# Kernel optimization log

Measured on AMD Instinct MI355X. Metric: run time of the kernel, lower is better.

Reference implementation:

```python
import jax, jax.numpy as jnp
import numpy as np
from jax import lax

B, C, H, W = 8, 64, 96, 96
OC = 64
KH = KW = 3
DG = 1
STRIDE = 1
PAD = 1
DIL = 1


def setup_inputs() -> dict:
    key = jax.random.key(0)
    k1, k2, k3, k4, k5 = jax.random.split(key, 5)
    x = jax.random.normal(k1, (B, C, H, W), jnp.float32)
    off_ch = DG * 3 * KH * KW
    # small random offset/mask conv params (the original inits them to zero,
    # which would make offsets degenerate; small values exercise the sampler)
    w_off = jax.random.normal(k2, (off_ch, C, KH, KW), jnp.float32) * 0.01
    b_off = jax.random.normal(k3, (off_ch,), jnp.float32) * 0.01
    stdv = 1.0 / float(np.sqrt(C * KH * KW))
    weight = jax.random.uniform(k4, (OC, C, KH, KW), jnp.float32, -stdv, stdv)
    bias = jax.random.uniform(k5, (OC,), jnp.float32, -stdv, stdv)
    return {"x": x, "w_off": w_off, "b_off": b_off, "weight": weight, "bias": bias}


def _deform_conv(x, w_off, b_off, weight, bias):
    Bt, Ct, Ht, Wt = x.shape
    K = KH * KW
    # standard conv producing offsets + mask logits
    om = lax.conv_general_dilated(
        x, w_off, (STRIDE, STRIDE), ((PAD, PAD), (PAD, PAD)),
        rhs_dilation=(DIL, DIL), dimension_numbers=("NCHW", "OIHW", "NCHW"),
    ) + b_off[None, :, None, None]
    o1, o2, m = jnp.split(om, 3, axis=1)  # each [B, DG*K, Ho, Wo]
    Ho, Wo = o1.shape[2], o1.shape[3]
    mask = jax.nn.sigmoid(m).reshape(Bt, DG, 1, K, Ho, Wo)
    off_y = o1.reshape(Bt, DG, K, Ho, Wo)
    off_x = o2.reshape(Bt, DG, K, Ho, Wo)
    # base sampling grid: p = out_pos*stride - pad + k*dilation + offset
    kk = jnp.arange(K)
    base_y = (kk // KW)[:, None] * DIL + (jnp.arange(Ho) * STRIDE - PAD)[None, :]  # [K, Ho]
    base_x = (kk % KW)[:, None] * DIL + (jnp.arange(Wo) * STRIDE - PAD)[None, :]   # [K, Wo]
    py = off_y + base_y[None, None, :, :, None].astype(x.dtype)  # [B, DG, K, Ho, Wo]
    px = off_x + base_x[None, None, :, None, :].astype(x.dtype)
    y0 = jnp.floor(py)
    x0 = jnp.floor(px)
    ly = py - y0
    lx = px - x0
    Cg = Ct // DG
    xg = x.reshape(Bt, DG, Cg, Ht * Wt)

    def gath(xf, idx):  # xf [Cg, H*W], idx [K*Ho*Wo]
        return jnp.take(xf, idx, axis=1)

    gather = jax.vmap(jax.vmap(gath))  # over B, DG

    sampled = jnp.zeros((Bt, DG, Cg, K, Ho, Wo), x.dtype)
    for dy, dx, wgt in ((0, 0, (1 - ly) * (1 - lx)), (0, 1, (1 - ly) * lx),
                        (1, 0, ly * (1 - lx)), (1, 1, ly * lx)):
        yy = y0 + dy
        xx = x0 + dx
        valid = (yy >= 0) & (yy < Ht) & (xx >= 0) & (xx < Wt)
        yi = jnp.clip(yy, 0, Ht - 1).astype(jnp.int32)
        xi = jnp.clip(xx, 0, Wt - 1).astype(jnp.int32)
        idx = (yi * Wt + xi).reshape(Bt, DG, K * Ho * Wo)
        v = gather(xg, idx).reshape(Bt, DG, Cg, K, Ho, Wo)
        sampled = sampled + v * (wgt * valid)[:, :, None]
    sampled = sampled * mask  # modulated
    wr = weight.reshape(OC, DG, Cg, K)
    out = jnp.einsum("bgckhw,ogck->bohw", sampled, wr) + bias[None, :, None, None]
    return out


def reference(x, w_off, b_off, weight, bias):
    return _deform_conv(x, w_off, b_off, weight, bias)
```

## Files before the change

### kernel.cpp

```cpp
#include <hip/hip_runtime.h>
#include <math.h>

#define Bn 8
#define Cn 64
#define Hn 96
#define Wn 96
#define HWn (Hn*Wn)
#define OCn 64
#define Kn 9
#define OFFCn 27
#define NPIX (Bn*HWn)
#define PGRPS (NPIX/64)
#define BLK_PER_B (HWn/64)

#define WPK1_N 15552
#define WPK2M_SHORTS 131072
#define WS_DWORDS (45*NPIX + WPK1_N + WPK2M_SHORTS/2)
#define WS_BYTES  ((size_t)WS_DWORDS*4)

typedef __attribute__((ext_vector_type(8))) short short8v;
typedef __attribute__((ext_vector_type(4))) float f32x4;

static __device__ __forceinline__ unsigned short bf16_rne(float f) {
    unsigned int u = __float_as_uint(f);
    return (unsigned short)((u + 0x7FFFu + ((u >> 16) & 1u)) >> 16);
}
static __device__ __forceinline__ float bf16_back(unsigned short h) {
    return __uint_as_float(((unsigned int)h) << 16);
}

__global__ __launch_bounds__(256) void dcn_wprep(
    const float* __restrict__ w_off,
    const float* __restrict__ weight,
    float* __restrict__ wpk1,
    short* __restrict__ wpk2m)
{
    const int g = blockIdx.x * 256 + threadIdx.x;
    if (g < WPK1_N) {
        const int c_all = g / 243;
        const int och   = (g % 243) / 9;
        const int ki    = g % 9;
        wpk1[g] = w_off[(och * 64 + c_all) * 9 + ki];
    }
    if (g < WPK2M_SHORTS / 8) {
        const int lane = g & 63;
        const int oct  = (g >> 6) & 3;
        const int c    = g >> 8;
        const int oc   = oct * 16 + (lane & 15);
        const float* wsrc = weight + (oc * 64 + c) * 9;
        short8v v;
#pragma unroll
        for (int j = 0; j < 8; ++j) {
            const int s = ((lane >> 4) & 3) * 8 + j;
            float f = 0.0f;
            if (s <= 8)                  f = wsrc[s];
            else if (s >= 16 && s <= 24) f = wsrc[s - 16];
            v[j] = (short)bf16_rne(f);
        }
        ((short8v*)wpk2m)[g] = v;
    }
}

__global__ __launch_bounds__(256, 2) void dcn_k1(
    const float* __restrict__ x,
    const float* __restrict__ wpk1,
    const float* __restrict__ b_off,
    float* __restrict__ pwbuf,
    int*   __restrict__ abuf)
{
    __shared__ float lds[4 * 64 * OFFCn];

    const int tid  = threadIdx.x;
    const int lane = tid & 63;
    const int wv   = tid >> 6;
    const int cbase = __builtin_amdgcn_readfirstlane(wv * 16);

    const int bid = (blockIdx.x & 7) * BLK_PER_B + (blockIdx.x >> 3);

    const int p  = bid * 64 + lane;
    const int b  = p / HWn;
    const int hw = p % HWn;
    const int ho = hw / Wn;
    const int wo = hw % Wn;

    const float* xb = x + b * (Cn * HWn);

    int   toff[Kn];
    float tval[Kn];
#pragma unroll
    for (int ki = 0; ki < Kn; ++ki) {
        const int yy = ho + ki / 3 - 1, xx = wo + ki % 3 - 1;
        const bool v = (yy >= 0) && (yy < Hn) && (xx >= 0) && (xx < Wn);
        toff[ki] = min(max(yy, 0), Hn - 1) * Wn + min(max(xx, 0), Wn - 1);
        tval[ki] = v ? 1.0f : 0.0f;
    }

    float om[OFFCn];
#pragma unroll
    for (int j = 0; j < OFFCn; ++j) om[j] = 0.0f;

    const float* wstream = wpk1 + cbase * 243;
    for (int ci = 0; ci < 16; ++ci) {
        const float* xc = xb + (cbase + ci) * HWn;
        float xk[Kn];
#pragma unroll
        for (int ki = 0; ki < Kn; ++ki)
            xk[ki] = xc[toff[ki]] * tval[ki];

        const float* wc = wstream + ci * 243;
#pragma unroll
        for (int och = 0; och < OFFCn; ++och) {
            const float* wp = wc + och * 9;
            float a = om[och];
#pragma unroll
            for (int ki = 0; ki < Kn; ++ki)
                a = fmaf(xk[ki], wp[ki], a);
            om[och] = a;
        }
    }

#pragma unroll
    for (int j = 0; j < OFFCn; ++j)
        lds[(wv * 64 + lane) * OFFCn + j] = om[j];
    __syncthreads();
#pragma unroll
    for (int j = 0; j < OFFCn; ++j) {
        float a = b_off[j];
#pragma unroll
        for (int ww = 0; ww < 4; ++ww)
            a += lds[(ww * 64 + lane) * OFFCn + j];
        om[j] = a;
    }

    float pw0[Kn], pw1[Kn], pw2[Kn], pw3[Kn];
    int   pav[Kn];
#pragma unroll
    for (int ki = 0; ki < Kn; ++ki) {
        const float py = om[ki]      + (float)(ki / 3 + ho - 1);
        const float px = om[Kn + ki] + (float)(ki % 3 + wo - 1);
        const float m  = 1.0f / (1.0f + __expf(-om[2 * Kn + ki]));

        const float y0f = floorf(py), x0f = floorf(px);
        const float ly = py - y0f, lx = px - x0f;
        const int iy0 = (int)y0f, ix0 = (int)x0f;
        const int iy1 = iy0 + 1,  ix1 = ix0 + 1;

        const float vy0 = (iy0 >= 0 && iy0 < Hn) ? 1.0f : 0.0f;
        const float vy1 = (iy1 >= 0 && iy1 < Hn) ? 1.0f : 0.0f;
        const float vx0 = (ix0 >= 0 && ix0 < Wn) ? 1.0f : 0.0f;
        const float vx1 = (ix1 >= 0 && ix1 < Wn) ? 1.0f : 0.0f;

        const int iy0c = min(max(iy0, 0), Hn - 1);
        const int iy1c = min(max(iy1, 0), Hn - 1);
        const int ix0c = min(max(ix0, 0), Wn - 1);
        const int ix1c = min(max(ix1, 0), Wn - 1);

        pw0[ki] = m * (1.0f - ly) * (1.0f - lx) * vy0 * vx0;
        pw1[ki] = m * (1.0f - ly) * lx          * vy0 * vx1;
        pw2[ki] = m * ly          * (1.0f - lx) * vy1 * vx0;
        pw3[ki] = m * ly          * lx          * vy1 * vx1;
        const int pa  = iy0c * Wn + ix0c;
        const int dx  = ix1c - ix0c;
        const int dyw = (iy1c - iy0c) * Wn;
        pav[ki] = pa | (dx << 16) | (dyw << 17);
    }

    if (wv == 0) {
#pragma unroll
        for (int ki = 0; ki < Kn; ++ki) pwbuf[(0 * Kn + ki) * NPIX + p] = pw0[ki];
#pragma unroll
        for (int ki = 0; ki < Kn; ++ki) abuf[ki * NPIX + p] = pav[ki];
    } else if (wv == 1) {
#pragma unroll
        for (int ki = 0; ki < Kn; ++ki) pwbuf[(1 * Kn + ki) * NPIX + p] = pw1[ki];
    } else if (wv == 2) {
#pragma unroll
        for (int ki = 0; ki < Kn; ++ki) pwbuf[(2 * Kn + ki) * NPIX + p] = pw2[ki];
    } else {
#pragma unroll
        for (int ki = 0; ki < Kn; ++ki) pwbuf[(3 * Kn + ki) * NPIX + p] = pw3[ki];
    }
}

__global__ __launch_bounds__(256, 2) void dcn_k2(
    const float* __restrict__ x,
    const short* __restrict__ wpk2m,
    const float* __restrict__ bias,
    const float* __restrict__ pwbuf,
    const int*   __restrict__ abuf,
    float* __restrict__ out)
{
    __shared__ short smp[32 * 64 * 8];

    const int tid  = threadIdx.x;
    const int lane = tid & 63;
    const int wv   = tid >> 6;

    const int bid = (blockIdx.x & 7) * BLK_PER_B + (blockIdx.x >> 3);

    const int p0  = bid * 64;
    const int b   = p0 / HWn;
    const int hwb = p0 % HWn;
    const int p   = p0 + lane;

    const float* xb = x + b * (Cn * HWn);

    float pw0[Kn], pw1[Kn], pw2[Kn], pw3[Kn];
    int   pav[Kn];
#pragma unroll
    for (int ki = 0; ki < Kn; ++ki) pw0[ki] = pwbuf[(0 * Kn + ki) * NPIX + p];
#pragma unroll
    for (int ki = 0; ki < Kn; ++ki) pw1[ki] = pwbuf[(1 * Kn + ki) * NPIX + p];
#pragma unroll
    for (int ki = 0; ki < Kn; ++ki) pw2[ki] = pwbuf[(2 * Kn + ki) * NPIX + p];
#pragma unroll
    for (int ki = 0; ki < Kn; ++ki) pw3[ki] = pwbuf[(3 * Kn + ki) * NPIX + p];
#pragma unroll
    for (int ki = 0; ki < Kn; ++ki) pav[ki] = abuf[ki * NPIX + p];

    f32x4 acc[4];
#pragma unroll
    for (int oct = 0; oct < 4; ++oct) acc[oct] = (f32x4){0.f, 0.f, 0.f, 0.f};

    const short8v* afrags = (const short8v*)wpk2m;

    for (int chunk = 0; chunk < 8; ++chunk) {
#pragma unroll
        for (int cc = 0; cc < 2; ++cc) {
            const int cl = (wv << 1) | cc;
            const float* xc = xb + (chunk * 8 + cl) * HWn;
            unsigned short hi[Kn], lo[Kn];
#pragma unroll
            for (int ki = 0; ki < Kn; ++ki) {
                const int av  = pav[ki];
                const int pa  = av & 0xFFFF;
                const int dx  = (av >> 16) & 1;
                const int dyw = av >> 17;
                const float* bp = xc + pa;
                const float v = pw0[ki] * bp[0] + pw1[ki] * bp[dx]
                              + pw2[ki] * bp[dyw] + pw3[ki] * bp[dyw + dx];
                hi[ki] = bf16_rne(v);
                lo[ki] = bf16_rne(v - bf16_back(hi[ki]));
            }
            short8v h0, h1, l0, l1;
#pragma unroll
            for (int j = 0; j < 8; ++j) { h0[j] = (short)hi[j]; l0[j] = (short)lo[j]; }
            h1 = (short8v){(short)hi[8], 0, 0, 0, 0, 0, 0, 0};
            l1 = (short8v){(short)lo[8], 0, 0, 0, 0, 0, 0, 0};
            const int r0 = cl * 4;
            *(short8v*)&smp[((r0 + 0) * 64 + lane) * 8] = h0;
            *(short8v*)&smp[((r0 + 1) * 64 + lane) * 8] = h1;
            *(short8v*)&smp[((r0 + 2) * 64 + lane) * 8] = l0;
            *(short8v*)&smp[((r0 + 3) * 64 + lane) * 8] = l1;
        }
        __syncthreads();

#pragma unroll
        for (int ks = 0; ks < 8; ++ks) {
            const short8v bfrag = *(const short8v*)
                &smp[((ks * 4 + (lane >> 4)) * 64 + wv * 16 + (lane & 15)) * 8];
#pragma unroll
            for (int oct = 0; oct < 4; ++oct) {
                const short8v afrag =
                    afrags[(((chunk * 8 + ks) * 4) + oct) * 64 + lane];
                acc[oct] = __builtin_amdgcn_mfma_f32_16x16x32_bf16(
                    afrag, bfrag, acc[oct], 0, 0, 0);
            }
        }
        __syncthreads();
    }

    const int pxl = wv * 16 + (lane & 15);
    float* ob = out + b * (OCn * HWn) + hwb + pxl;
#pragma unroll
    for (int oct = 0; oct < 4; ++oct) {
#pragma unroll
        for (int r = 0; r < 4; ++r) {
            const int oc = oct * 16 + ((lane >> 4) & 3) * 4 + r;
            ob[oc * HWn] = acc[oct][r] + bias[oc];
        }
    }
}

__global__ __launch_bounds__(64) void dcn_r1(
    const float* __restrict__ x,
    const float* __restrict__ w_off,
    const float* __restrict__ b_off,
    const float* __restrict__ weight,
    const float* __restrict__ bias,
    float* __restrict__ out)
{
    const int p  = blockIdx.x * 64 + threadIdx.x;
    const int b  = p / HWn;
    const int hw = p % HWn;
    const int ho = hw / Wn;
    const int wo = hw % Wn;
    const float* xb = x + b * (Cn * HWn);

    float om[OFFCn];
#pragma unroll
    for (int j = 0; j < OFFCn; ++j) om[j] = b_off[j];

    int   toff[Kn];
    float tval[Kn];
#pragma unroll
    for (int ki = 0; ki < Kn; ++ki) {
        const int yy = ho + ki / 3 - 1, xx = wo + ki % 3 - 1;
        const bool v = (yy >= 0) && (yy < Hn) && (xx >= 0) && (xx < Wn);
        toff[ki] = min(max(yy, 0), Hn - 1) * Wn + min(max(xx, 0), Wn - 1);
        tval[ki] = v ? 1.0f : 0.0f;
    }
    for (int c = 0; c < Cn; ++c) {
        const float* xc = xb + c * HWn;
        float xk[Kn];
#pragma unroll
        for (int ki = 0; ki < Kn; ++ki) xk[ki] = xc[toff[ki]] * tval[ki];
        const float* wc = w_off + c * Kn;
#pragma unroll
        for (int och = 0; och < OFFCn; ++och) {
            const float* wp = wc + och * (Cn * Kn);
            float a = om[och];
#pragma unroll
            for (int ki = 0; ki < Kn; ++ki) a = fmaf(xk[ki], wp[ki], a);
            om[och] = a;
        }
    }
    float pw0[Kn], pw1[Kn], pw2[Kn], pw3[Kn];
    int   pa[Kn], pdx[Kn], pdyw[Kn];
#pragma unroll
    for (int ki = 0; ki < Kn; ++ki) {
        const float py = om[ki]      + (float)(ki / 3 + ho - 1);
        const float px = om[Kn + ki] + (float)(ki % 3 + wo - 1);
        const float m  = 1.0f / (1.0f + __expf(-om[2 * Kn + ki]));
        const float y0f = floorf(py), x0f = floorf(px);
        const float ly = py - y0f, lx = px - x0f;
        const int iy0 = (int)y0f, ix0 = (int)x0f;
        const int iy1 = iy0 + 1,  ix1 = ix0 + 1;
        const float vy0 = (iy0 >= 0 && iy0 < Hn) ? 1.0f : 0.0f;
        const float vy1 = (iy1 >= 0 && iy1 < Hn) ? 1.0f : 0.0f;
        const float vx0 = (ix0 >= 0 && ix0 < Wn) ? 1.0f : 0.0f;
        const float vx1 = (ix1 >= 0 && ix1 < Wn) ? 1.0f : 0.0f;
        const int iy0c = min(max(iy0, 0), Hn - 1);
        const int iy1c = min(max(iy1, 0), Hn - 1);
        const int ix0c = min(max(ix0, 0), Wn - 1);
        const int ix1c = min(max(ix1, 0), Wn - 1);
        pw0[ki] = m * (1.0f - ly) * (1.0f - lx) * vy0 * vx0;
        pw1[ki] = m * (1.0f - ly) * lx          * vy0 * vx1;
        pw2[ki] = m * ly          * (1.0f - lx) * vy1 * vx0;
        pw3[ki] = m * ly          * lx          * vy1 * vx1;
        pa[ki]   = iy0c * Wn + ix0c;
        pdx[ki]  = ix1c - ix0c;
        pdyw[ki] = (iy1c - iy0c) * Wn;
    }
    float acc[OCn];
#pragma unroll
    for (int oc = 0; oc < OCn; ++oc) acc[oc] = bias[oc];
    for (int c = 0; c < Cn; ++c) {
        const float* xc = xb + c * HWn;
        float s[Kn];
#pragma unroll
        for (int ki = 0; ki < Kn; ++ki) {
            const float* bp = xc + pa[ki];
            s[ki] = pw0[ki] * bp[0] + pw1[ki] * bp[pdx[ki]]
                  + pw2[ki] * bp[pdyw[ki]] + pw3[ki] * bp[pdyw[ki] + pdx[ki]];
        }
        const float* wc = weight + c * Kn;
#pragma unroll
        for (int oc = 0; oc < OCn; ++oc) {
            const float* wp = wc + oc * (Cn * Kn);
            float a = acc[oc];
#pragma unroll
            for (int ki = 0; ki < Kn; ++ki) a = fmaf(s[ki], wp[ki], a);
            acc[oc] = a;
        }
    }
    float* ob = out + b * (OCn * HWn) + hw;
#pragma unroll
    for (int oc = 0; oc < OCn; ++oc) ob[oc * HWn] = acc[oc];
}

extern "C" void kernel_launch(void* const* d_in, const int* in_sizes, int n_in,
                              void* d_out, int out_size, void* d_ws, size_t ws_size,
                              hipStream_t stream) {
    const float* x      = (const float*)d_in[0];
    const float* w_off  = (const float*)d_in[1];
    const float* b_off  = (const float*)d_in[2];
    const float* weight = (const float*)d_in[3];
    const float* bias   = (const float*)d_in[4];
    float* out = (float*)d_out;

    if (ws_size >= WS_BYTES) {
        float* pwbuf = (float*)d_ws;
        int*   abuf  = (int*)((float*)d_ws + 36 * NPIX);
        float* wpk1  = (float*)d_ws + 45 * NPIX;
        short* wpk2m = (short*)(wpk1 + WPK1_N);
        hipLaunchKernelGGL(dcn_wprep, dim3(64), dim3(256), 0, stream,
                           w_off, weight, wpk1, wpk2m);
        hipLaunchKernelGGL(dcn_k1, dim3(PGRPS), dim3(256), 0, stream,
                           x, wpk1, b_off, pwbuf, abuf);
        hipLaunchKernelGGL(dcn_k2, dim3(PGRPS), dim3(256), 0, stream,
                           x, wpk2m, bias, pwbuf, abuf, out);
    } else {
        hipLaunchKernelGGL(dcn_r1, dim3(NPIX / 64), dim3(64), 0, stream,
                           x, w_off, b_off, weight, bias, out);
    }
}
```

Measured before the change: 237.3 us.

## Restructure deform-conv GEMM kernel to per-wave private LDS tiles without block barriers

```diff
diff --git a/kernel.cpp b/kernel.cpp
--- a/kernel.cpp
+++ b/kernel.cpp
@@ -19,6 +19,7 @@
 #define WS_BYTES  ((size_t)WS_DWORDS*4)
 
 typedef __attribute__((ext_vector_type(8))) short short8v;
+typedef __attribute__((ext_vector_type(4))) short short4v;
 typedef __attribute__((ext_vector_type(4))) float f32x4;
 
 static __device__ __forceinline__ unsigned short bf16_rne(float f) {
@@ -182,7 +183,7 @@
     }
 }
 
-__global__ __launch_bounds__(256, 2) void dcn_k2(
+__global__ __launch_bounds__(128, 2) void dcn_k2w(
     const float* __restrict__ x,
     const short* __restrict__ wpk2m,
     const float* __restrict__ bias,
@@ -190,94 +191,147 @@
     const int*   __restrict__ abuf,
     float* __restrict__ out)
 {
-    __shared__ short smp[32 * 64 * 8];
+    __shared__ short smp[2 * 2 * 2048];
 
     const int tid  = threadIdx.x;
     const int lane = tid & 63;
     const int wv   = tid >> 6;
+    const int q    = lane >> 5;
+    const int px   = lane & 31;
+    const int kb   = q * 4;
 
     const int bid = (blockIdx.x & 7) * BLK_PER_B + (blockIdx.x >> 3);
-
-    const int p0  = bid * 64;
+    const int p0  = bid * 64 + wv * 32;
     const int b   = p0 / HWn;
     const int hwb = p0 % HWn;
-    const int p   = p0 + lane;
+    const int p   = p0 + px;
 
     const float* xb = x + b * (Cn * HWn);
-
-    float pw0[Kn], pw1[Kn], pw2[Kn], pw3[Kn];
-    int   pav[Kn];
-#pragma unroll
-    for (int ki = 0; ki < Kn; ++ki) pw0[ki] = pwbuf[(0 * Kn + ki) * NPIX + p];
-#pragma unroll
-    for (int ki = 0; ki < Kn; ++ki) pw1[ki] = pwbuf[(1 * Kn + ki) * NPIX + p];
-#pragma unroll
-    for (int ki = 0; ki < Kn; ++ki) pw2[ki] = pwbuf[(2 * Kn + ki) * NPIX + p];
-#pragma unroll
-    for (int ki = 0; ki < Kn; ++ki) pw3[ki] = pwbuf[(3 * Kn + ki) * NPIX + p];
-#pragma unroll
-    for (int ki = 0; ki < Kn; ++ki) pav[ki] = abuf[ki * NPIX + p];
-
-    f32x4 acc[4];
-#pragma unroll
-    for (int oct = 0; oct < 4; ++oct) acc[oct] = (f32x4){0.f, 0.f, 0.f, 0.f};
+    short* myA = smp + wv * 4096;
+    short* myB = myA + 2048;
+
+    {
+        short8v z = (short8v){0, 0, 0, 0, 0, 0, 0, 0};
+#pragma unroll
+        for (int t = 0; t < 2; ++t) {
+            const int idx = t * 64 + lane;
+            const int r   = 1 + 2 * (idx >> 5);
+            const int pp  = idx & 31;
+            *(short8v*)&myA[(r * 32 + pp) * 8] = z;
+            *(short8v*)&myB[(r * 32 + pp) * 8] = z;
+        }
+    }
+
+    float pw0[5], pw1[5], pw2[5], pw3[5];
+    int   pav[5];
+#pragma unroll
+    for (int i = 0; i < 5; ++i) pw0[i] = pwbuf[(0 * Kn + kb + i) * NPIX + p];
+#pragma unroll
+    for (int i = 0; i < 5; ++i) pw1[i] = pwbuf[(1 * Kn + kb + i) * NPIX + p];
+#pragma unroll
+    for (int i = 0; i < 5; ++i) pw2[i] = pwbuf[(2 * Kn + kb + i) * NPIX + p];
+#pragma unroll
+    for (int i = 0; i < 5; ++i) pw3[i] = pwbuf[(3 * Kn + kb + i) * NPIX + p];
+#pragma unroll
+    for (int i = 0; i < 5; ++i) pav[i] = abuf[(kb + i) * NPIX + p];
+
+    f32x4 acc[2][4];
+#pragma unroll
+    for (int t = 0; t < 2; ++t)
+#pragma unroll
+        for (int oct = 0; oct < 4; ++oct)
+            acc[t][oct] = (f32x4){0.f, 0.f, 0.f, 0.f};
 
     const short8v* afrags = (const short8v*)wpk2m;
-
-    for (int chunk = 0; chunk < 8; ++chunk) {
-#pragma unroll
-        for (int cc = 0; cc < 2; ++cc) {
-            const int cl = (wv << 1) | cc;
-            const float* xc = xb + (chunk * 8 + cl) * HWn;
-            unsigned short hi[Kn], lo[Kn];
-#pragma unroll
-            for (int ki = 0; ki < Kn; ++ki) {
-                const int av  = pav[ki];
+    const int r4  = lane >> 4;
+    const int c16 = lane & 15;
+
+    for (int it = 0; it < 16; ++it) {
+        const int ch0 = it * 4;
+
+#pragma unroll
+        for (int c = 0; c < 2; ++c) {
+            const float* xc = xb + (ch0 + c) * HWn;
+            unsigned short h[5], l[5];
+#pragma unroll
+            for (int i = 0; i < 5; ++i) {
+                const int av  = pav[i];
                 const int pa  = av & 0xFFFF;
                 const int dx  = (av >> 16) & 1;
                 const int dyw = av >> 17;
                 const float* bp = xc + pa;
-                const float v = pw0[ki] * bp[0] + pw1[ki] * bp[dx]
-                              + pw2[ki] * bp[dyw] + pw3[ki] * bp[dyw + dx];
-                hi[ki] = bf16_rne(v);
-                lo[ki] = bf16_rne(v - bf16_back(hi[ki]));
+                const float v = pw0[i] * bp[0] + pw1[i] * bp[dx]
+                              + pw2[i] * bp[dyw] + pw3[i] * bp[dyw + dx];
+                h[i] = bf16_rne(v);
+                l[i] = bf16_rne(v - bf16_back(h[i]));
             }
-            short8v h0, h1, l0, l1;
-#pragma unroll
-            for (int j = 0; j < 8; ++j) { h0[j] = (short)hi[j]; l0[j] = (short)lo[j]; }
-            h1 = (short8v){(short)hi[8], 0, 0, 0, 0, 0, 0, 0};
-            l1 = (short8v){(short)lo[8], 0, 0, 0, 0, 0, 0, 0};
-            const int r0 = cl * 4;
-            *(short8v*)&smp[((r0 + 0) * 64 + lane) * 8] = h0;
-            *(short8v*)&smp[((r0 + 1) * 64 + lane) * 8] = h1;
-            *(short8v*)&smp[((r0 + 2) * 64 + lane) * 8] = l0;
-            *(short8v*)&smp[((r0 + 3) * 64 + lane) * 8] = l1;
-        }
-        __syncthreads();
-
-#pragma unroll
-        for (int ks = 0; ks < 8; ++ks) {
-            const short8v bfrag = *(const short8v*)
-                &smp[((ks * 4 + (lane >> 4)) * 64 + wv * 16 + (lane & 15)) * 8];
+            short4v h4 = (short4v){(short)h[0], (short)h[1], (short)h[2], (short)h[3]};
+            short4v l4 = (short4v){(short)l[0], (short)l[1], (short)l[2], (short)l[3]};
+            *(short4v*)&myA[((c * 4 + 0) * 32 + px) * 8 + q * 4] = h4;
+            *(short4v*)&myA[((c * 4 + 2) * 32 + px) * 8 + q * 4] = l4;
+            myA[((c * 4 + 0 + q) * 32 + px) * 8 + (q ? 0 : 4)] = (short)h[4];
+            myA[((c * 4 + 2 + q) * 32 + px) * 8 + (q ? 0 : 4)] = (short)l[4];
+        }
+
+#pragma unroll
+        for (int c = 0; c < 2; ++c) {
+            const float* xc = xb + (ch0 + 2 + c) * HWn;
+            unsigned short h[5], l[5];
+#pragma unroll
+            for (int i = 0; i < 5; ++i) {
+                const int av  = pav[i];
+                const int pa  = av & 0xFFFF;
+                const int dx  = (av >> 16) & 1;
+                const int dyw = av >> 17;
+                const float* bp = xc + pa;
+                const float v = pw0[i] * bp[0] + pw1[i] * bp[dx]
+                              + pw2[i] * bp[dyw] + pw3[i] * bp[dyw + dx];
+                h[i] = bf16_rne(v);
+                l[i] = bf16_rne(v - bf16_back(h[i]));
+            }
+            short4v h4 = (short4v){(short)h[0], (short)h[1], (short)h[2], (short)h[3]};
+            short4v l4 = (short4v){(short)l[0], (short)l[1], (short)l[2], (short)l[3]};
+            *(short4v*)&myB[((c * 4 + 0) * 32 + px) * 8 + q * 4] = h4;
+            *(short4v*)&myB[((c * 4 + 2) * 32 + px) * 8 + q * 4] = l4;
+            myB[((c * 4 + 0 + q) * 32 + px) * 8 + (q ? 0 : 4)] = (short)h[4];
+            myB[((c * 4 + 2 + q) * 32 + px) * 8 + (q ? 0 : 4)] = (short)l[4];
+        }
+
+#pragma unroll
+        for (int c = 0; c < 2; ++c) {
+            const short8v bf0 = *(const short8v*)&myA[((c * 4 + r4) * 32 + c16) * 8];
+            const short8v bf1 = *(const short8v*)&myA[((c * 4 + r4) * 32 + 16 + c16) * 8];
 #pragma unroll
             for (int oct = 0; oct < 4; ++oct) {
-                const short8v afrag =
-                    afrags[(((chunk * 8 + ks) * 4) + oct) * 64 + lane];
-                acc[oct] = __builtin_amdgcn_mfma_f32_16x16x32_bf16(
-                    afrag, bfrag, acc[oct], 0, 0, 0);
+                const short8v af = afrags[(((ch0 + c) * 4) + oct) * 64 + lane];
+                acc[0][oct] = __builtin_amdgcn_mfma_f32_16x16x32_bf16(af, bf0, acc[0][oct], 0, 0, 0);
+                acc[1][oct] = __builtin_amdgcn_mfma_f32_16x16x32_bf16(af, bf1, acc[1][oct], 0, 0, 0);
             }
         }
-        __syncthreads();
-    }
-
-    const int pxl = wv * 16 + (lane & 15);
-    float* ob = out + b * (OCn * HWn) + hwb + pxl;
-#pragma unroll
-    for (int oct = 0; oct < 4; ++oct) {
-#pragma unroll
-        for (int r = 0; r < 4; ++r) {
-            const int oc = oct * 16 + ((lane >> 4) & 3) * 4 + r;
-            ob[oc * HWn] = acc[oct][r] + bias[oc];
+
+#pragma unroll
+        for (int c = 0; c < 2; ++c) {
+            const short8v bf0 = *(const short8v*)&myB[((c * 4 + r4) * 32 + c16) * 8];
+            const short8v bf1 = *(const short8v*)&myB[((c * 4 + r4) * 32 + 16 + c16) * 8];
+#pragma unroll
+            for (int oct = 0; oct < 4; ++oct) {
+                const short8v af = afrags[(((ch0 + 2 + c) * 4) + oct) * 64 + lane];
+                acc[0][oct] = __builtin_amdgcn_mfma_f32_16x16x32_bf16(af, bf0, acc[0][oct], 0, 0, 0);
+                acc[1][oct] = __builtin_amdgcn_mfma_f32_16x16x32_bf16(af, bf1, acc[1][oct], 0, 0, 0);
+            }
+        }
+    }
+
+#pragma unroll
+    for (int t = 0; t < 2; ++t) {
+        float* ob = out + b * (OCn * HWn) + hwb + t * 16 + c16;
+#pragma unroll
+        for (int oct = 0; oct < 4; ++oct) {
+#pragma unroll
+            for (int r = 0; r < 4; ++r) {
+                const int oc = oct * 16 + r4 * 4 + r;
+                ob[oc * HWn] = acc[t][oct][r] + bias[oc];
+            }
         }
     }
 }
@@ -398,7 +452,7 @@
                            w_off, weight, wpk1, wpk2m);
         hipLaunchKernelGGL(dcn_k1, dim3(PGRPS), dim3(256), 0, stream,
                            x, wpk1, b_off, pwbuf, abuf);
-        hipLaunchKernelGGL(dcn_k2, dim3(PGRPS), dim3(256), 0, stream,
+        hipLaunchKernelGGL(dcn_k2w, dim3(PGRPS), dim3(128), 0, stream,
                            x, wpk2m, bias, pwbuf, abuf, out);
     } else {
         hipLaunchKernelGGL(dcn_r1, dim3(NPIX / 64), dim3(64), 0, stream,
```

Measured after the change: 231.0 us (median of 2 runs). 1.03x faster.
